# Kernel tuning notes

Measured on AMD Instinct MI355X. Metric: run time of the kernel, lower is better.

## Reference

```python
import jax, jax.numpy as jnp
import numpy as np

EPS = 1e-5

def conv2d(x, w, padding):
    # x: (N, Cin, H, W), w: (Cout, Cin, kh, kw)
    return jax.lax.conv_general_dilated(
        x, w, window_strides=(1, 1),
        padding=[(padding, padding), (padding, padding)],
        dimension_numbers=('NCHW', 'OIHW', 'NCHW'))

def proj_bn_relu(x, w, gamma, beta, mean, var):
    # 1x1 conv + BatchNorm (eval mode, running stats) + ReLU
    y = conv2d(x, w, 0)
    scale = (gamma / jnp.sqrt(var + EPS))[None, :, None, None]
    shift = (beta - mean * gamma / jnp.sqrt(var + EPS))[None, :, None, None]
    return jax.nn.relu(y * scale + shift)

def setup_inputs() -> dict:
    key = jax.random.key(0)
    ks = jax.random.split(key, 16)
    B, Sx, Sy, C1, C2, Co, H, W, K = 2, 4, 4, 64, 64, 64, 128, 128, 3
    inp = {
        'u': jax.random.normal(ks[0], (B, Sx, C1, H, W), jnp.float32),
        'v': jax.random.normal(ks[1], (B, Sy, C2, H, W), jnp.float32),
        'pu_w': jax.random.normal(ks[2], (C1, C1, 1, 1), jnp.float32) * 0.05,
        'pu_gamma': jnp.ones((C1,), jnp.float32),
        'pu_beta': jnp.zeros((C1,), jnp.float32),
        'pu_mean': jax.random.normal(ks[3], (C1,), jnp.float32) * 0.1,
        'pu_var': jax.random.uniform(ks[4], (C1,), jnp.float32, 0.5, 1.5),
        'pv_w': jax.random.normal(ks[5], (C2, C2, 1, 1), jnp.float32) * 0.05,
        'pv_gamma': jnp.ones((C2,), jnp.float32),
        'pv_beta': jnp.zeros((C2,), jnp.float32),
        'pv_mean': jax.random.normal(ks[6], (C2,), jnp.float32) * 0.1,
        'pv_var': jax.random.uniform(ks[7], (C2,), jnp.float32, 0.5, 1.5),
        'conv_w': jax.random.normal(ks[8], (Co, C1 + C2, K, K), jnp.float32) * 0.02,
        'conv_b': jax.random.normal(ks[9], (Co,), jnp.float32) * 0.02,
    }
    return inp

def reference(u, v, pu_w, pu_gamma, pu_beta, pu_mean, pu_var,
              pv_w, pv_gamma, pv_beta, pv_mean, pv_var, conv_w, conv_b):
    B, Sx, C1, H, W = u.shape
    _, Sy, C2, _, _ = v.shape
    pad = 1
    # flatten set dims into batch for the 1x1 proj+BN+ReLU
    uf = proj_bn_relu(u.reshape(B * Sx, C1, H, W), pu_w, pu_gamma, pu_beta, pu_mean, pu_var)
    vf = proj_bn_relu(v.reshape(B * Sy, C2, H, W), pv_w, pv_gamma, pv_beta, pv_mean, pv_var)
    # conv over concat channels is linear -> split weight and broadcast-add,
    # exactly equal to conv(cat(repeat(u), repeat(v))) without materializing
    # the (B,Sx,Sy,C1+C2,H,W) tensor.
    w_u = conv_w[:, :C1]   # (Co, C1, K, K)
    w_v = conv_w[:, C1:]   # (Co, C2, K, K)
    ou = conv2d(uf, w_u, pad)  # (B*Sx, Co, Ho, Wo)
    ov = conv2d(vf, w_v, pad)  # (B*Sy, Co, Ho, Wo)
    Co, Ho, Wo = ou.shape[1], ou.shape[2], ou.shape[3]
    ou = ou.reshape(B, Sx, 1, Co, Ho, Wo)
    ov = ov.reshape(B, 1, Sy, Co, Ho, Wo)
    out = ou + ov + conv_b[None, None, None, :, None, None]
    return out  # (B, Sx, Sy, Co, Ho, Wo)
```

## Files before the change

kernel.cpp:

```cpp
#include <hip/hip_runtime.h>
#include <hip/hip_bf16.h>

#define C   64
#define Hh  128
#define Ww  128
#define HW  16384

typedef __attribute__((ext_vector_type(8))) short bf16x8;
typedef __attribute__((ext_vector_type(4))) float f32x4;

__device__ __forceinline__ unsigned short f2bf(float f) {
    unsigned u = __builtin_bit_cast(unsigned, f);
    unsigned r = (u + 0x7fff + ((u >> 16) & 1)) >> 16;
    return (unsigned short)r;
}

__global__ __launch_bounds__(256, 3) void proj_mfma(
    const float* __restrict__ xu, const float* __restrict__ xv,
    const float* __restrict__ pu_w, const float* __restrict__ pu_g,
    const float* __restrict__ pu_b, const float* __restrict__ pu_m,
    const float* __restrict__ pu_v,
    const float* __restrict__ pv_w, const float* __restrict__ pv_g,
    const float* __restrict__ pv_b, const float* __restrict__ pv_m,
    const float* __restrict__ pv_v,
    const float* __restrict__ conv_w,
    short* __restrict__ wpu, short* __restrict__ wpv,
    short* __restrict__ yu, short* __restrict__ yv)
{
    __shared__ short xs[256 * 64];
    __shared__ short pwl[64 * 72];
    __shared__ float ssh[64];

    const int img16 = blockIdx.y;
    const int sel   = img16 >> 3;
    const int img   = img16 & 7;
    const float* x  = sel ? xv   : xu;
    const float* pw = sel ? pv_w : pu_w;
    const float* pg = sel ? pv_g : pu_g;
    const float* pb = sel ? pv_b : pu_b;
    const float* pm = sel ? pv_m : pu_m;
    const float* pv = sel ? pv_v : pu_v;
    short* y        = sel ? yv   : yu;

    const int pix0 = blockIdx.x * 256;
    const int tid  = threadIdx.x;

    for (int e = tid; e < 2048; e += 256) {
        const int co = e >> 5;
        const int ci0 = (e & 31) * 2;
        const float scale = pg[co] * rsqrtf(pv[co] + 1e-5f);
        const int packed = (int)f2bf(pw[co * 64 + ci0] * scale)
                         | ((int)f2bf(pw[co * 64 + ci0 + 1] * scale) << 16);
        *(int*)&pwl[co * 72 + ci0] = packed;
    }
    if (tid < 64) {
        const float scale = pg[tid] * rsqrtf(pv[tid] + 1e-5f);
        ssh[tid] = pb[tid] - pm[tid] * scale;
    }

    const float* xb = x + (size_t)img * C * HW;
    const int qd = tid & 63;
    const int cp = tid >> 6;
#pragma unroll
    for (int kk = 0; kk < 2; ++kk) {
        int4 pk[4];
#pragma unroll
        for (int k4 = 0; k4 < 4; ++k4) {
            const int ci0 = (cp * 8 + kk * 4 + k4) * 2;
            const f32x4 a = *(const f32x4*)&xb[(size_t)ci0 * HW + pix0 + qd * 4];
            const f32x4 b = *(const f32x4*)&xb[(size_t)(ci0 + 1) * HW + pix0 + qd * 4];
#pragma unroll
            for (int j = 0; j < 4; ++j) {
                const int packed = (int)f2bf(a[j]) | ((int)f2bf(b[j]) << 16);
                if (k4 == 0) pk[j].x = packed;
                else if (k4 == 1) pk[j].y = packed;
                else if (k4 == 2) pk[j].z = packed;
                else pk[j].w = packed;
            }
        }
        const int chunk = cp * 2 + kk;
#pragma unroll
        for (int j = 0; j < 4; ++j) {
            const int px = qd * 4 + j;
            *(int4*)&xs[px * 64 + ((chunk ^ (px & 7)) << 3)] = pk[j];
        }
    }
    __syncthreads();

    const int wq = tid >> 6;
    const int lane = tid & 63;
    const int lx = lane & 15;
    const int q  = lane >> 4;

    f32x4 acc[4][4];
#pragma unroll
    for (int mt = 0; mt < 4; ++mt)
#pragma unroll
        for (int nt = 0; nt < 4; ++nt) acc[mt][nt] = (f32x4){0.f, 0.f, 0.f, 0.f};

#pragma unroll
    for (int kc = 0; kc < 2; ++kc) {
        bf16x8 a[4], b[4];
#pragma unroll
        for (int mt = 0; mt < 4; ++mt) {
            const int px = (wq * 4 + mt) * 16 + lx;
            a[mt] = *(const bf16x8*)&xs[px * 64 + (((kc * 4 + q) ^ (lx & 7)) << 3)];
        }
#pragma unroll
        for (int nt = 0; nt < 4; ++nt)
            b[nt] = *(const bf16x8*)&pwl[(nt * 16 + lx) * 72 + kc * 32 + q * 8];
#pragma unroll
        for (int mt = 0; mt < 4; ++mt)
#pragma unroll
            for (int nt = 0; nt < 4; ++nt)
                acc[mt][nt] = __builtin_amdgcn_mfma_f32_16x16x32_bf16(a[mt], b[nt], acc[mt][nt], 0, 0, 0);
    }

    __syncthreads();
#pragma unroll
    for (int mt = 0; mt < 4; ++mt)
#pragma unroll
        for (int nt = 0; nt < 4; ++nt)
#pragma unroll
            for (int r = 0; r < 4; ++r) {
                const int px = (wq * 4 + mt) * 16 + q * 4 + r;
                const int co = nt * 16 + lx;
                float vv = acc[mt][nt][r] + ssh[co];
                vv = fmaxf(vv, 0.f);
                xs[px * 64 + (co ^ ((px & 7) << 3))] = (short)f2bf(vv);
            }
    __syncthreads();
    short* yo = y + ((size_t)img * HW + pix0) * C;
#pragma unroll
    for (int it = 0; it < 8; ++it) {
        const int idx = tid + it * 256;
        const int oct = idx & 7, px = idx >> 3;
        *(int4*)&yo[(size_t)px * C + oct * 8] =
            *(const int4*)&xs[px * 64 + ((oct ^ (px & 7)) << 3)];
    }

    if (img16 < 2) {
        short* wpx = img16 ? wpv : wpu;
        const int c = img16;
        for (int idx = blockIdx.x * 256 + tid; idx < 36864; idx += 64 * 256) {
            const int ci = idx & 31;
            const int co = (idx >> 5) & 63;
            const int r3 = idx >> 11;
            const int tap = r3 % 9;
            const int ch  = r3 / 9;
            const float src = conv_w[(size_t)(co * 128 + c * 64 + ch * 32 + ci) * 9 + tap];
            wpx[idx] = (short)f2bf(src);
        }
    }
}

template<bool FUSED>
__global__ __launch_bounds__(128, 2) void conv_fused(
    const short* __restrict__ act, const short* __restrict__ wp,
    const float* __restrict__ oug, const float* __restrict__ bias,
    float* __restrict__ outp)
{
    __shared__ short xs[204 * 72];
    __shared__ float ts[16 * 132];
    __shared__ float sbias[64];

    const int img = blockIdx.y;
    const int tx = blockIdx.x & 3, ty = blockIdx.x >> 2;
    const int h0 = ty * 4, w0 = tx * 32;
    const int tid = threadIdx.x;
    const int wq = tid >> 6;
    const int lane = tid & 63;
    const int lx = lane & 15;
    const int q  = lane >> 4;
    const int q8 = q * 8;

    if (FUSED && tid < 64) sbias[tid] = bias[tid];

    const short* ub = act + (size_t)img * HW * C;
    for (int idx = tid; idx < 1632; idx += 128) {
        const int oct = idx & 7;
        const int cell = idx >> 3;
        const int h = cell / 34, w = cell - h * 34;
        const int gh = h0 - 1 + h, gw = w0 - 1 + w;
        int4 v = {0, 0, 0, 0};
        if (gh >= 0 && gh < Hh && gw >= 0 && gw < Ww)
            v = *(const int4*)&ub[(size_t)(gh * Ww + gw) * C + oct * 8];
        *(int4*)(&xs[cell * 72 + oct * 8]) = v;
    }
    __syncthreads();

    f32x4 acc[4][4];
#pragma unroll
    for (int mt = 0; mt < 4; ++mt)
#pragma unroll
        for (int nt = 0; nt < 4; ++nt) acc[mt][nt] = (f32x4){0.f, 0.f, 0.f, 0.f};

#pragma unroll
    for (int ch = 0; ch < 2; ++ch)
#pragma unroll
        for (int t = 0; t < 9; ++t) {
            const int ky = t / 3;
            const int kx = t - ky * 3;
            bf16x8 a[4], b[4];
#pragma unroll
            for (int mt = 0; mt < 4; ++mt)
                a[mt] = *(const bf16x8*)&wp[(((ch * 9 + t) * 64) + mt * 16 + lx) * 32 + q8];
#pragma unroll
            for (int nt = 0; nt < 4; ++nt) {
                const int cell = (2 * wq + (nt >> 1) + ky) * 34 + (nt & 1) * 16 + lx + kx;
                b[nt] = *(const bf16x8*)&xs[cell * 72 + ch * 32 + q8];
            }
#pragma unroll
            for (int mt = 0; mt < 4; ++mt)
#pragma unroll
                for (int nt = 0; nt < 4; ++nt)
                    acc[mt][nt] = __builtin_amdgcn_mfma_f32_16x16x32_bf16(a[mt], b[nt], acc[mt][nt], 0, 0, 0);
        }

    if (FUSED) {
#pragma unroll
        for (int mt = 0; mt < 4; ++mt)
#pragma unroll
            for (int nt = 0; nt < 4; ++nt)
#pragma unroll
                for (int r = 0; r < 4; ++r)
                    acc[mt][nt][r] += sbias[mt * 16 + q * 4 + r];
    }

    const int b  = img >> 2;
    const int sy = img & 3;

#pragma unroll
    for (int mt = 0; mt < 4; ++mt) {
        __syncthreads();
#pragma unroll
        for (int nt = 0; nt < 4; ++nt)
#pragma unroll
            for (int r = 0; r < 4; ++r)
                ts[(q * 4 + r) * 132 + (2 * wq + (nt >> 1)) * 32 + (nt & 1) * 16 + lx]
                    = acc[mt][nt][r];
        __syncthreads();
        if (!FUSED) {
            float* ob = outp + (size_t)img * C * HW;
#pragma unroll
            for (int k = 0; k < 4; ++k) {
                const int f = tid + k * 128;
                const int co = f >> 5, c2 = f & 31;
                const int px = c2 * 4;
                const int h2 = px >> 5, w2 = px & 31;
                *(f32x4*)&ob[(size_t)(mt * 16 + co) * HW + (h0 + h2) * Ww + w0 + w2] =
                    *(const f32x4*)&ts[co * 132 + c2 * 4];
            }
        } else {
#pragma unroll
            for (int k = 0; k < 4; ++k) {
                const int f = tid + k * 128;
                const int co = f >> 5, c2 = f & 31;
                const int px = c2 * 4;
                const int h2 = px >> 5, w2 = px & 31;
                const size_t off = (size_t)(mt * 16 + co) * HW + (h0 + h2) * Ww + w0 + w2;
                const f32x4 tv = *(const f32x4*)&ts[co * 132 + c2 * 4];
#pragma unroll
                for (int sx = 0; sx < 4; ++sx) {
                    const f32x4 o = *(const f32x4*)&oug[(size_t)(b * 4 + sx) * C * HW + off];
                    f32x4 rr = tv + o;
                    __builtin_nontemporal_store(rr,
                        (f32x4*)&outp[((size_t)((b * 4 + sx) * 4 + sy)) * C * HW + off]);
                }
            }
        }
    }
}

extern "C" void kernel_launch(void* const* d_in, const int* in_sizes, int n_in,
                              void* d_out, int out_size, void* d_ws, size_t ws_size,
                              hipStream_t stream)
{
    const float* u        = (const float*)d_in[0];
    const float* v        = (const float*)d_in[1];
    const float* pu_w     = (const float*)d_in[2];
    const float* pu_gamma = (const float*)d_in[3];
    const float* pu_beta  = (const float*)d_in[4];
    const float* pu_mean  = (const float*)d_in[5];
    const float* pu_var   = (const float*)d_in[6];
    const float* pv_w     = (const float*)d_in[7];
    const float* pv_gamma = (const float*)d_in[8];
    const float* pv_beta  = (const float*)d_in[9];
    const float* pv_mean  = (const float*)d_in[10];
    const float* pv_var   = (const float*)d_in[11];
    const float* conv_w   = (const float*)d_in[12];
    const float* conv_b   = (const float*)d_in[13];
    float* out = (float*)d_out;

    char* ws = (char*)d_ws;
    short* uf  = (short*)(ws);
    short* vf  = (short*)(ws + 16777216);
    float* ou  = (float*)(ws + 33554432);
    char*  aux = ws + 67108864;
    short* wpu = (short*)(aux);
    short* wpv = (short*)(aux + 73728);

    dim3 gp(64, 16);
    proj_mfma<<<gp, 256, 0, stream>>>(u, v,
                                      pu_w, pu_gamma, pu_beta, pu_mean, pu_var,
                                      pv_w, pv_gamma, pv_beta, pv_mean, pv_var,
                                      conv_w, wpu, wpv, uf, vf);

    dim3 gc(128, 8);
    conv_fused<false><<<gc, 128, 0, stream>>>(uf, wpu, nullptr, nullptr, ou);
    conv_fused<true ><<<gc, 128, 0, stream>>>(vf, wpv, ou, conv_b, out);
}
```

Baseline: 258.9 us.

## Fuse u and v 3x3 convs into one cross-product kernel per tile

Replaces the two conv launches (u conv writing an fp32 intermediate, then v conv reading it back for the broadcast add) with a single kernel. Each 512-thread block loads all 8 activation tiles (4 u, 4 v) of a 2x32 pixel strip into XOR-swizzled LDS, and each wave computes one image's conv. The results are staged in LDS and all 16 sx/sy combinations are written directly. This removes the fp32 ou round trip through global memory and one launch, at the cost of large LDS use (about 140KB), so only one block fits per CU, and the tile is smaller (2 rows).

Measured after the change: 264.4 us. 2.1% more time.

```diff
diff --git a/kernel.cpp b/kernel.cpp
--- a/kernel.cpp
+++ b/kernel.cpp
@@ -154,40 +154,45 @@
     }
 }
 
-template<bool FUSED>
-__global__ __launch_bounds__(128, 2) void conv_fused(
-    const short* __restrict__ act, const short* __restrict__ wp,
-    const float* __restrict__ oug, const float* __restrict__ bias,
-    float* __restrict__ outp)
+__global__ __launch_bounds__(512, 1) void conv_cross(
+    const short* __restrict__ uf, const short* __restrict__ vf,
+    const short* __restrict__ wpu, const short* __restrict__ wpv,
+    const float* __restrict__ bias, float* __restrict__ outp)
 {
-    __shared__ short xs[204 * 72];
-    __shared__ float ts[16 * 132];
+    __shared__ short xh[8][136 * 64];
     __shared__ float sbias[64];
 
-    const int img = blockIdx.y;
+    const int b  = blockIdx.y;
     const int tx = blockIdx.x & 3, ty = blockIdx.x >> 2;
-    const int h0 = ty * 4, w0 = tx * 32;
+    const int h0 = ty * 2, w0 = tx * 32;
     const int tid = threadIdx.x;
-    const int wq = tid >> 6;
+    const int wq  = tid >> 6;
+    const int side = wq >> 2;
     const int lane = tid & 63;
     const int lx = lane & 15;
     const int q  = lane >> 4;
     const int q8 = q * 8;
 
-    if (FUSED && tid < 64) sbias[tid] = bias[tid];
-
-    const short* ub = act + (size_t)img * HW * C;
-    for (int idx = tid; idx < 1632; idx += 128) {
-        const int oct = idx & 7;
-        const int cell = idx >> 3;
-        const int h = cell / 34, w = cell - h * 34;
-        const int gh = h0 - 1 + h, gw = w0 - 1 + w;
-        int4 v = {0, 0, 0, 0};
-        if (gh >= 0 && gh < Hh && gw >= 0 && gw < Ww)
-            v = *(const int4*)&ub[(size_t)(gh * Ww + gw) * C + oct * 8];
-        *(int4*)(&xs[cell * 72 + oct * 8]) = v;
-    }
-    __syncthreads();
+    if (tid < 64) sbias[tid] = bias[tid];
+
+#pragma unroll
+    for (int ii = 0; ii < 8; ++ii) {
+        const short* ab = (ii < 4 ? uf : vf) + (size_t)(b * 4 + (ii & 3)) * HW * C;
+        for (int idx2 = tid; idx2 < 1088; idx2 += 512) {
+            const int oct = idx2 & 7;
+            const int cell = idx2 >> 3;
+            const int h = cell / 34, w = cell - h * 34;
+            const int gh = h0 - 1 + h, gw = w0 - 1 + w;
+            int4 v = {0, 0, 0, 0};
+            if (gh >= 0 && gh < Hh && gw >= 0 && gw < Ww)
+                v = *(const int4*)&ab[(size_t)(gh * Ww + gw) * C + oct * 8];
+            *(int4*)&xh[ii][cell * 64 + ((oct ^ (cell & 7)) << 3)] = v;
+        }
+    }
+    __syncthreads();
+
+    const short* wp = side ? wpv : wpu;
+    const short* myh = &xh[wq][0];
 
     f32x4 acc[4][4];
 #pragma unroll
@@ -201,73 +206,56 @@
         for (int t = 0; t < 9; ++t) {
             const int ky = t / 3;
             const int kx = t - ky * 3;
-            bf16x8 a[4], b[4];
+            bf16x8 a[4], bfr[4];
 #pragma unroll
             for (int mt = 0; mt < 4; ++mt)
                 a[mt] = *(const bf16x8*)&wp[(((ch * 9 + t) * 64) + mt * 16 + lx) * 32 + q8];
 #pragma unroll
             for (int nt = 0; nt < 4; ++nt) {
-                const int cell = (2 * wq + (nt >> 1) + ky) * 34 + (nt & 1) * 16 + lx + kx;
-                b[nt] = *(const bf16x8*)&xs[cell * 72 + ch * 32 + q8];
+                const int cell = ((nt >> 1) + ky) * 34 + (nt & 1) * 16 + lx + kx;
+                bfr[nt] = *(const bf16x8*)&myh[cell * 64 + (((ch * 4 + q) ^ (cell & 7)) << 3)];
             }
 #pragma unroll
             for (int mt = 0; mt < 4; ++mt)
 #pragma unroll
                 for (int nt = 0; nt < 4; ++nt)
-                    acc[mt][nt] = __builtin_amdgcn_mfma_f32_16x16x32_bf16(a[mt], b[nt], acc[mt][nt], 0, 0, 0);
-        }
-
-    if (FUSED) {
-#pragma unroll
-        for (int mt = 0; mt < 4; ++mt)
-#pragma unroll
-            for (int nt = 0; nt < 4; ++nt)
-#pragma unroll
-                for (int r = 0; r < 4; ++r)
-                    acc[mt][nt][r] += sbias[mt * 16 + q * 4 + r];
-    }
-
-    const int b  = img >> 2;
-    const int sy = img & 3;
-
-#pragma unroll
-    for (int mt = 0; mt < 4; ++mt) {
-        __syncthreads();
+                    acc[mt][nt] = __builtin_amdgcn_mfma_f32_16x16x32_bf16(a[mt], bfr[nt], acc[mt][nt], 0, 0, 0);
+        }
+
+    __syncthreads();
+    float* slab = (float*)&xh[0][0];
+    float* ms = slab + wq * 4352;
+#pragma unroll
+    for (int mt = 0; mt < 4; ++mt)
 #pragma unroll
         for (int nt = 0; nt < 4; ++nt)
 #pragma unroll
-            for (int r = 0; r < 4; ++r)
-                ts[(q * 4 + r) * 132 + (2 * wq + (nt >> 1)) * 32 + (nt & 1) * 16 + lx]
-                    = acc[mt][nt][r];
-        __syncthreads();
-        if (!FUSED) {
-            float* ob = outp + (size_t)img * C * HW;
-#pragma unroll
-            for (int k = 0; k < 4; ++k) {
-                const int f = tid + k * 128;
-                const int co = f >> 5, c2 = f & 31;
-                const int px = c2 * 4;
-                const int h2 = px >> 5, w2 = px & 31;
-                *(f32x4*)&ob[(size_t)(mt * 16 + co) * HW + (h0 + h2) * Ww + w0 + w2] =
-                    *(const f32x4*)&ts[co * 132 + c2 * 4];
-            }
-        } else {
-#pragma unroll
-            for (int k = 0; k < 4; ++k) {
-                const int f = tid + k * 128;
-                const int co = f >> 5, c2 = f & 31;
-                const int px = c2 * 4;
-                const int h2 = px >> 5, w2 = px & 31;
-                const size_t off = (size_t)(mt * 16 + co) * HW + (h0 + h2) * Ww + w0 + w2;
-                const f32x4 tv = *(const f32x4*)&ts[co * 132 + c2 * 4];
-#pragma unroll
-                for (int sx = 0; sx < 4; ++sx) {
-                    const f32x4 o = *(const f32x4*)&oug[(size_t)(b * 4 + sx) * C * HW + off];
-                    f32x4 rr = tv + o;
-                    __builtin_nontemporal_store(rr,
-                        (f32x4*)&outp[((size_t)((b * 4 + sx) * 4 + sy)) * C * HW + off]);
-                }
-            }
+            for (int r = 0; r < 4; ++r) {
+                const int co = mt * 16 + q * 4 + r;
+                const int px = (nt >> 1) * 32 + (nt & 1) * 16 + lx;
+                float vv = acc[mt][nt][r];
+                if (side) vv += sbias[co];
+                ms[co * 68 + px] = vv;
+            }
+    __syncthreads();
+
+#pragma unroll
+    for (int cc2 = 0; cc2 < 2; ++cc2) {
+        const int cc = wq * 2 + cc2;
+        const int sx = cc >> 2, sy = cc & 3;
+        const float* us = slab + sx * 4352;
+        const float* vs = slab + (4 + sy) * 4352;
+        float* ob = outp + ((size_t)((b * 4 + sx) * 4 + sy)) * C * HW;
+        const int h2 = lx >> 3;
+        const int w2 = (lx & 7) * 4;
+        const size_t pixoff = (size_t)(h0 + h2) * Ww + w0 + w2;
+#pragma unroll
+        for (int pass = 0; pass < 16; ++pass) {
+            const int co = pass * 4 + q;
+            const f32x4 a = *(const f32x4*)&us[co * 68 + lx * 4];
+            const f32x4 c = *(const f32x4*)&vs[co * 68 + lx * 4];
+            f32x4 rr = a + c;
+            __builtin_nontemporal_store(rr, (f32x4*)&ob[(size_t)co * HW + pixoff]);
         }
     }
 }
@@ -295,8 +283,7 @@
     char* ws = (char*)d_ws;
     short* uf  = (short*)(ws);
     short* vf  = (short*)(ws + 16777216);
-    float* ou  = (float*)(ws + 33554432);
-    char*  aux = ws + 67108864;
+    char*  aux = ws + 33554432;
     short* wpu = (short*)(aux);
     short* wpv = (short*)(aux + 73728);
 
@@ -306,7 +293,6 @@
                                       pv_w, pv_gamma, pv_beta, pv_mean, pv_var,
                                       conv_w, wpu, wpv, uf, vf);
 
-    dim3 gc(128, 8);
-    conv_fused<false><<<gc, 128, 0, stream>>>(uf, wpu, nullptr, nullptr, ou);
-    conv_fused<true ><<<gc, 128, 0, stream>>>(vf, wpv, ou, conv_b, out);
-}
+    dim3 gcv(256, 2);
+    conv_cross<<<gcv, 512, 0, stream>>>(uf, vf, wpu, wpv, conv_b, out);
+}
```
